# Kernel optimization log

Hardware: AMD Instinct MI355X
Metric: run time of the kernel (lower is better)

## Reference

```python
import jax, jax.numpy as jnp
import numpy as np

DEPTH, DIM, HEADS, EXP = 6, 768, 12, 4
B, N = 8, 1024
EPS = 1e-5


def setup_inputs() -> dict:
    key = jax.random.key(0)
    ks = jax.random.split(key, 6)
    s = 0.02
    inp = {
        "x": jax.random.normal(ks[0], (B, N, DIM), dtype=jnp.float32),
        "ln1_g": jnp.ones((DEPTH, DIM), jnp.float32),
        "ln1_b": jnp.zeros((DEPTH, DIM), jnp.float32),
        "wqkv": jax.random.normal(ks[1], (DEPTH, DIM, 3 * DIM), jnp.float32) * s,
        "bqkv": jnp.zeros((DEPTH, 3 * DIM), jnp.float32),
        "ln2_g": jnp.ones((DEPTH, DIM), jnp.float32),
        "ln2_b": jnp.zeros((DEPTH, DIM), jnp.float32),
        "w1": jax.random.normal(ks[2], (DEPTH, DIM, EXP * DIM), jnp.float32) * s,
        "b1": jnp.zeros((DEPTH, EXP * DIM), jnp.float32),
        "w2": jax.random.normal(ks[3], (DEPTH, EXP * DIM, DIM), jnp.float32) * s,
        "b2": jnp.zeros((DEPTH, DIM), jnp.float32),
    }
    return inp


def _layernorm(x, g, b):
    mu = jnp.mean(x, axis=-1, keepdims=True)
    var = jnp.mean(jnp.square(x - mu), axis=-1, keepdims=True)
    return (x - mu) * jax.lax.rsqrt(var + EPS) * g + b


def _block(x, p):
    ln1_g, ln1_b, wqkv, bqkv, ln2_g, ln2_b, w1, b1, w2, b2 = p
    # --- attention (pre-norm, residual) ---
    x1 = _layernorm(x, ln1_g, ln1_b)
    qkv = x1 @ wqkv + bqkv  # [b, n, 3*dim]
    q, k, v = jnp.split(qkv, 3, axis=-1)
    dh = DIM // HEADS
    def heads(t):  # b n (h d) -> b h n d
        return t.reshape(B, N, HEADS, dh).transpose(0, 2, 1, 3)
    q, k, v = heads(q), heads(k), heads(v)
    scale = DIM ** (-0.5)  # NB: module scales by full dim, not head dim
    dots = jnp.einsum("bhnd,bhmd->bhnm", q, k) * scale
    attn = jax.nn.softmax(dots, axis=-1)
    out = jnp.einsum("bhnm,bhmd->bhnd", attn, v)
    out = out.transpose(0, 2, 1, 3).reshape(B, N, DIM)
    x = x + out
    # --- feedforward (pre-norm, residual) ---
    x2 = _layernorm(x, ln2_g, ln2_b)
    h = jax.nn.gelu(x2 @ w1 + b1, approximate=False)
    x = x + (h @ w2 + b2)
    return x


def reference(x, ln1_g, ln1_b, wqkv, bqkv, ln2_g, ln2_b, w1, b1, w2, b2):
    params = (ln1_g, ln1_b, wqkv, bqkv, ln2_g, ln2_b, w1, b1, w2, b2)

    def body(carry, p):
        return _block(carry, p), None

    x, _ = jax.lax.scan(body, x, params)
    return x
```

## Files before the change

### kernel.cpp

```cpp
#include <hip/hip_runtime.h>
#include <hip/hip_bf16.h>
#include <math.h>

#define DEPTH 6
#define DIM   768
#define HEADS 12
#define DH    64
#define NCTX  1024
#define BATCH 8
#define ROWS  (BATCH*NCTX)
#define DIM3  (3*DIM)
#define DIMF  (4*DIM)
#define LNEPS 1e-5f

typedef __attribute__((ext_vector_type(8))) short short8;
typedef __attribute__((ext_vector_type(4))) float floatx4;
using bf16 = __hip_bfloat16;

static __device__ __forceinline__ bf16 f2bf(float v){ return __float2bfloat16(v); }
static __device__ __forceinline__ float bf2f(unsigned short u){
    union { unsigned int i; float f; } c; c.i = ((unsigned int)u) << 16; return c.f;
}
static __device__ __forceinline__ unsigned short bfu(float v){ return __bfloat16_as_ushort(f2bf(v)); }

static __device__ __forceinline__ void gl_lds16(const void* g, void* l) {
    __builtin_amdgcn_global_load_lds((const __attribute__((address_space(1))) void*)g,
                                     (__attribute__((address_space(3))) void*)l, 16, 0, 0);
}

__global__ void k_transpose_convert(const float* __restrict__ W, bf16* __restrict__ WT,
                                    int K, int N) {
    __shared__ float tile[32][33];
    int l = blockIdx.z;
    const float* Wl = W + (size_t)l * K * N;
    bf16* WTl = WT + (size_t)l * K * N;
    int n0 = blockIdx.x * 32, k0 = blockIdx.y * 32;
    int tx = threadIdx.x, ty = threadIdx.y;
#pragma unroll
    for (int i = 0; i < 4; i++)
        tile[ty + i*8][tx] = Wl[(size_t)(k0 + ty + i*8) * N + n0 + tx];
    __syncthreads();
#pragma unroll
    for (int i = 0; i < 4; i++)
        WTl[(size_t)(n0 + ty + i*8) * K + k0 + tx] = f2bf(tile[tx][ty + i*8]);
}

__global__ __launch_bounds__(256) void k_layernorm(const float* __restrict__ x,
                                                   const float* __restrict__ g,
                                                   const float* __restrict__ b,
                                                   bf16* __restrict__ y) {
    int row  = blockIdx.x * 4 + (threadIdx.x >> 6);
    int lane = threadIdx.x & 63;
    const float4* xr = (const float4*)(x + (size_t)row * DIM);
    float4 v[3];
    float s = 0.f, s2 = 0.f;
#pragma unroll
    for (int i = 0; i < 3; i++) {
        v[i] = xr[lane + i*64];
        s  += v[i].x + v[i].y + v[i].z + v[i].w;
        s2 += v[i].x*v[i].x + v[i].y*v[i].y + v[i].z*v[i].z + v[i].w*v[i].w;
    }
#pragma unroll
    for (int m = 1; m < 64; m <<= 1) { s += __shfl_xor(s, m); s2 += __shfl_xor(s2, m); }
    float mu  = s * (1.f / DIM);
    float var = s2 * (1.f / DIM) - mu * mu;
    float rs  = rsqrtf(var + LNEPS);
    bf16* yr = y + (size_t)row * DIM;
    const float4* g4 = (const float4*)g;
    const float4* b4 = (const float4*)b;
#pragma unroll
    for (int i = 0; i < 3; i++) {
        float4 gg = g4[lane + i*64], bb = b4[lane + i*64];
        float r0 = (v[i].x - mu) * rs * gg.x + bb.x;
        float r1 = (v[i].y - mu) * rs * gg.y + bb.y;
        float r2 = (v[i].z - mu) * rs * gg.z + bb.z;
        float r3 = (v[i].w - mu) * rs * gg.w + bb.w;
        unsigned int lo = bfu(r0) | ((unsigned int)bfu(r1) << 16);
        unsigned int hi = bfu(r2) | ((unsigned int)bfu(r3) << 16);
        uint2 u; u.x = lo; u.y = hi;
        *(uint2*)&yr[4 * (lane + i*64)] = u;
    }
}

template<int MODE>
__global__ __launch_bounds__(256) void k_gemm(const bf16* __restrict__ A,
                                              const bf16* __restrict__ WT,
                                              const float* __restrict__ bias,
                                              bf16* __restrict__ outb,
                                              float* __restrict__ outf,
                                              int N, int K) {
    __shared__ __align__(16) bf16 As[2][128*32];
    __shared__ __align__(16) bf16 Bs[2][128*32];
    int nt = N >> 7;
    int nwg = gridDim.x;
    int fblk = blockIdx.x;
    int swz = (fblk & 7) * (nwg >> 3) + (fblk >> 3);
    int m0 = (swz / nt) * 128, n0 = (swz % nt) * 128;
    int t = threadIdx.x;
    int lane = t & 63, w = t >> 6;
    int wr = (w >> 1) * 64, wc = (w & 1) * 64;
    int lr = lane & 15, lg = lane >> 4;
    int c0 = t, c1 = 256 + t;
    int r0g = c0 >> 2, e0 = (c0 & 3) * 8;
    int r1g = c1 >> 2, e1 = (c1 & 3) * 8;
    const bf16* Arow0 = A  + (size_t)(m0 + r0g) * K + e0;
    const bf16* Arow1 = A  + (size_t)(m0 + r1g) * K + e1;
    const bf16* Brow0 = WT + (size_t)(n0 + r0g) * K + e0;
    const bf16* Brow1 = WT + (size_t)(n0 + r1g) * K + e1;

    floatx4 acc[4][4] = {};
    int NT = K >> 5;
    gl_lds16(Arow0, &As[0][c0 * 8]);
    gl_lds16(Brow0, &Bs[0][c0 * 8]);
    gl_lds16(Arow1, &As[0][c1 * 8]);
    gl_lds16(Brow1, &Bs[0][c1 * 8]);
    __syncthreads();
    int cur = 0;
    for (int ks = 0; ks < NT; ks++) {
        if (ks + 1 < NT) {
            int ko = (ks + 1) << 5;
            gl_lds16(Arow0 + ko, &As[cur^1][c0 * 8]);
            gl_lds16(Brow0 + ko, &Bs[cur^1][c0 * 8]);
            gl_lds16(Arow1 + ko, &As[cur^1][c1 * 8]);
            gl_lds16(Brow1 + ko, &Bs[cur^1][c1 * 8]);
        }
        short8 af[4], bfr[4];
#pragma unroll
        for (int i = 0; i < 4; i++) af[i]  = *(const short8*)&As[cur][(wr + i*16 + lr)*32 + lg*8];
#pragma unroll
        for (int j = 0; j < 4; j++) bfr[j] = *(const short8*)&Bs[cur][(wc + j*16 + lr)*32 + lg*8];
#pragma unroll
        for (int i = 0; i < 4; i++)
#pragma unroll
            for (int j = 0; j < 4; j++)
                acc[i][j] = __builtin_amdgcn_mfma_f32_16x16x32_bf16(af[i], bfr[j], acc[i][j], 0, 0, 0);
        __syncthreads();
        cur ^= 1;
    }
#pragma unroll
    for (int i = 0; i < 4; i++)
#pragma unroll
        for (int j = 0; j < 4; j++)
#pragma unroll
            for (int r = 0; r < 4; r++) {
                int row = m0 + wr + i*16 + lg*4 + r;
                int col = n0 + wc + j*16 + lr;
                float vv = acc[i][j][r] + bias[col];
                if (MODE == 0) {
                    outb[(size_t)row * N + col] = f2bf(vv);
                } else if (MODE == 1) {
                    float u = 1.5957691216f * (vv + 0.044715f * vv * vv * vv);
                    float gs = 1.f / (1.f + __expf(-u));
                    outb[(size_t)row * N + col] = f2bf(vv * gs);
                } else {
                    outf[(size_t)row * N + col] += vv;
                }
            }
}

static __device__ __forceinline__ int vt_off(int d, int k) {
    int dw = d * 36 + (k >> 1);
    dw ^= (d & 0x38) >> 1;
    return dw * 2 + (k & 1);
}

__global__ __launch_bounds__(256, 3) void k_attn(const bf16* __restrict__ qkv,
                                                 float* __restrict__ x) {
    int f = blockIdx.x;
    int b  = f & 7;
    int rr = f >> 3;
    int h  = rr % 12;
    int qt = rr / 12;
    int t = threadIdx.x, lane = t & 63, w = t >> 6;
    int lr = lane & 15, lg = lane >> 4;
    const size_t bn0 = (size_t)b * NCTX;
    const bf16* Qg = qkv + bn0 * DIM3 + h * DH;
    const bf16* Kg = Qg + DIM;
    const bf16* Vg = Qg + 2 * DIM;
    int q0 = qt * 128 + w * 32;

    const float qs = 0.036084391824351615f * 1.4426950408889634f;
    short8 qf[2][2];
#pragma unroll
    for (int i = 0; i < 2; i++)
#pragma unroll
        for (int s = 0; s < 2; s++) {
            short8 raw = *(const short8*)&Qg[(size_t)(q0 + i*16 + lr) * DIM3 + s*32 + lg*8];
            short8 o;
#pragma unroll
            for (int e = 0; e < 8; e++)
                o[e] = (short)bfu(bf2f((unsigned short)raw[e]) * qs);
            qf[i][s] = o;
        }

    __shared__ __align__(16) bf16 Ks[64][72];
    __shared__ __align__(16) bf16 VTs[64 * 72];
    __shared__ __align__(16) bf16 Ps[4][32][72];

    int sr[2], sc[2];
#pragma unroll
    for (int it = 0; it < 2; it++) { int c = it*256 + t; sr[it] = c >> 3; sc[it] = (c & 7) * 8; }

    floatx4 oacc[2][4] = {};
    float mrow[2][4], lrow[2][4];
#pragma unroll
    for (int i = 0; i < 2; i++)
#pragma unroll
        for (int r = 0; r < 4; r++) { mrow[i][r] = -1e30f; lrow[i][r] = 0.f; }

    uint4 kreg[2], vreg[2];
#pragma unroll
    for (int it = 0; it < 2; it++) {
        kreg[it] = *(const uint4*)&Kg[(size_t)sr[it] * DIM3 + sc[it]];
        vreg[it] = *(const uint4*)&Vg[(size_t)sr[it] * DIM3 + sc[it]];
    }

    for (int kt = 0; kt < 16; kt++) {
        __syncthreads();
#pragma unroll
        for (int it = 0; it < 2; it++) {
            *(uint4*)&Ks[sr[it]][sc[it]] = kreg[it];
            const bf16* vp = (const bf16*)&vreg[it];
#pragma unroll
            for (int e = 0; e < 8; e++) VTs[vt_off(sc[it] + e, sr[it])] = vp[e];
        }
        __syncthreads();
        if (kt + 1 < 16) {
            int kv0 = (kt + 1) * 64;
#pragma unroll
            for (int it = 0; it < 2; it++) {
                kreg[it] = *(const uint4*)&Kg[(size_t)(kv0 + sr[it]) * DIM3 + sc[it]];
                vreg[it] = *(const uint4*)&Vg[(size_t)(kv0 + sr[it]) * DIM3 + sc[it]];
            }
        }

        floatx4 sacc[2][4] = {};
#pragma unroll
        for (int j = 0; j < 4; j++) {
            short8 kf0 = *(const short8*)&Ks[j*16 + lr][lg*8];
            short8 kf1 = *(const short8*)&Ks[j*16 + lr][32 + lg*8];
#pragma unroll
            for (int i = 0; i < 2; i++) {
                sacc[i][j] = __builtin_amdgcn_mfma_f32_16x16x32_bf16(qf[i][0], kf0, sacc[i][j], 0, 0, 0);
                sacc[i][j] = __builtin_amdgcn_mfma_f32_16x16x32_bf16(qf[i][1], kf1, sacc[i][j], 0, 0, 0);
            }
        }

#pragma unroll
        for (int i = 0; i < 2; i++)
#pragma unroll
            for (int r = 0; r < 4; r++) {
                float mx = fmaxf(fmaxf(sacc[i][0][r], sacc[i][1][r]),
                                 fmaxf(sacc[i][2][r], sacc[i][3][r]));
#pragma unroll
                for (int m = 1; m < 16; m <<= 1) mx = fmaxf(mx, __shfl_xor(mx, m));
                if (mx > mrow[i][r] + 8.f) {
                    float corr = exp2f(mrow[i][r] - mx);
                    mrow[i][r] = mx;
                    lrow[i][r] *= corr;
#pragma unroll
                    for (int j = 0; j < 4; j++) oacc[i][j][r] *= corr;
                }
                float sum = 0.f;
#pragma unroll
                for (int j = 0; j < 4; j++) {
                    float pv = exp2f(sacc[i][j][r] - mrow[i][r]);
                    sum += pv;
                    Ps[w][i*16 + lg*4 + r][j*16 + lr] = f2bf(pv);
                }
#pragma unroll
                for (int m = 1; m < 16; m <<= 1) sum += __shfl_xor(sum, m);
                lrow[i][r] += sum;
            }

#pragma unroll
        for (int s = 0; s < 2; s++) {
            short8 pa[2];
#pragma unroll
            for (int i = 0; i < 2; i++) pa[i] = *(const short8*)&Ps[w][i*16 + lr][s*32 + lg*8];
#pragma unroll
            for (int j = 0; j < 4; j++) {
                short8 vb = *(const short8*)&VTs[vt_off(j*16 + lr, s*32 + lg*8)];
#pragma unroll
                for (int i = 0; i < 2; i++)
                    oacc[i][j] = __builtin_amdgcn_mfma_f32_16x16x32_bf16(pa[i], vb, oacc[i][j], 0, 0, 0);
            }
        }
    }

    float* xr = x + bn0 * DIM + (size_t)h * DH;
#pragma unroll
    for (int i = 0; i < 2; i++)
#pragma unroll
        for (int j = 0; j < 4; j++)
#pragma unroll
            for (int r = 0; r < 4; r++) {
                int row = q0 + i*16 + lg*4 + r;
                int col = j*16 + lr;
                xr[(size_t)row * DIM + col] += oacc[i][j][r] / lrow[i][r];
            }
}

extern "C" void kernel_launch(void* const* d_in, const int* in_sizes, int n_in,
                              void* d_out, int out_size, void* d_ws, size_t ws_size,
                              hipStream_t stream) {
    const float* x_in  = (const float*)d_in[0];
    const float* ln1_g = (const float*)d_in[1];
    const float* ln1_b = (const float*)d_in[2];
    const float* wqkv  = (const float*)d_in[3];
    const float* bqkv  = (const float*)d_in[4];
    const float* ln2_g = (const float*)d_in[5];
    const float* ln2_b = (const float*)d_in[6];
    const float* w1    = (const float*)d_in[7];
    const float* b1    = (const float*)d_in[8];
    const float* w2    = (const float*)d_in[9];
    const float* b2    = (const float*)d_in[10];
    float* x = (float*)d_out;

    char* ws = (char*)d_ws;
    size_t off = 0;
    auto alloc = [&](size_t bytes) { void* p = ws + off; off += (bytes + 255) & ~255ull; return p; };
    bf16* wqkvT = (bf16*)alloc((size_t)DEPTH * DIM * DIM3 * 2);
    bf16* w1T   = (bf16*)alloc((size_t)DEPTH * DIM * DIMF * 2);
    bf16* w2T   = (bf16*)alloc((size_t)DEPTH * DIMF * DIM * 2);
    bf16* xn    = (bf16*)alloc((size_t)ROWS * DIM * 2);
    bf16* qkvh  = (bf16*)alloc((size_t)ROWS * DIMF * 2);
    if (off > ws_size) return;

    hipMemcpyAsync(x, x_in, (size_t)ROWS * DIM * 4, hipMemcpyDeviceToDevice, stream);

    k_transpose_convert<<<dim3(DIM3/32, DIM/32,  DEPTH), dim3(32, 8), 0, stream>>>(wqkv, wqkvT, DIM,  DIM3);
    k_transpose_convert<<<dim3(DIMF/32, DIM/32,  DEPTH), dim3(32, 8), 0, stream>>>(w1,   w1T,   DIM,  DIMF);
    k_transpose_convert<<<dim3(DIM/32,  DIMF/32, DEPTH), dim3(32, 8), 0, stream>>>(w2,   w2T,   DIMF, DIM);

    for (int l = 0; l < DEPTH; l++) {
        k_layernorm<<<ROWS/4, 256, 0, stream>>>(x, ln1_g + l*DIM, ln1_b + l*DIM, xn);
        k_gemm<0><<<dim3((DIM3/128)*(ROWS/128)), 256, 0, stream>>>(
            xn, wqkvT + (size_t)l*DIM*DIM3, bqkv + (size_t)l*DIM3, qkvh, nullptr, DIM3, DIM);
        k_attn<<<dim3(768), 256, 0, stream>>>(qkvh, x);
        k_layernorm<<<ROWS/4, 256, 0, stream>>>(x, ln2_g + l*DIM, ln2_b + l*DIM, xn);
        k_gemm<1><<<dim3((DIMF/128)*(ROWS/128)), 256, 0, stream>>>(
            xn, w1T + (size_t)l*DIM*DIMF, b1 + (size_t)l*DIMF, qkvh, nullptr, DIMF, DIM);
        k_gemm<2><<<dim3((DIM/128)*(ROWS/128)), 256, 0, stream>>>(
            qkvh, w2T + (size_t)l*DIMF*DIM, b2 + (size_t)l*DIM, nullptr, x, DIM, DIMF);
    }
}
```

Before: 1.785 ms.

## Rewrite attention with 32x32x16 MFMA and transposed score layout

Moves the flash-attention kernel from 16x16x32 MFMA tiles to 32x32x16 tiles. It computes S^T (K as the A operand) so each lane owns one query column, which cuts the row max and sum reductions to a single cross-half shuffle. K and P are stored in XOR-swizzled LDS to avoid bank conflicts. The online-softmax correction factors are broadcast through a small shared buffer so they can be applied to the output accumulator layout. This adds LDS traffic and layout complexity, and it relies on intra-wave ordering of the shared writes and reads with no barrier.

Measured after the change: 1.648 ms. -7.7%, faster.

```diff
diff --git a/kernel.cpp b/kernel.cpp
--- a/kernel.cpp
+++ b/kernel.cpp
@@ -13,15 +13,20 @@
 #define DIMF  (4*DIM)
 #define LNEPS 1e-5f
 
-typedef __attribute__((ext_vector_type(8))) short short8;
-typedef __attribute__((ext_vector_type(4))) float floatx4;
+typedef __attribute__((ext_vector_type(8)))  short short8;
+typedef __attribute__((ext_vector_type(4)))  float floatx4;
+typedef __attribute__((ext_vector_type(16))) float floatx16;
 using bf16 = __hip_bfloat16;
+typedef unsigned int u32;
 
 static __device__ __forceinline__ bf16 f2bf(float v){ return __float2bfloat16(v); }
 static __device__ __forceinline__ float bf2f(unsigned short u){
     union { unsigned int i; float f; } c; c.i = ((unsigned int)u) << 16; return c.f;
 }
 static __device__ __forceinline__ unsigned short bfu(float v){ return __bfloat16_as_ushort(f2bf(v)); }
+static __device__ __forceinline__ u32 pk2(float a, float b){
+    return (u32)bfu(a) | ((u32)bfu(b) << 16);
+}
 
 static __device__ __forceinline__ void gl_lds16(const void* g, void* l) {
     __builtin_amdgcn_global_load_lds((const __attribute__((address_space(1))) void*)g,
@@ -75,9 +80,7 @@
         float r1 = (v[i].y - mu) * rs * gg.y + bb.y;
         float r2 = (v[i].z - mu) * rs * gg.z + bb.z;
         float r3 = (v[i].w - mu) * rs * gg.w + bb.w;
-        unsigned int lo = bfu(r0) | ((unsigned int)bfu(r1) << 16);
-        unsigned int hi = bfu(r2) | ((unsigned int)bfu(r3) << 16);
-        uint2 u; u.x = lo; u.y = hi;
+        uint2 u; u.x = pk2(r0, r1); u.y = pk2(r2, r3);
         *(uint2*)&yr[4 * (lane + i*64)] = u;
     }
 }
@@ -172,7 +175,7 @@
     int h  = rr % 12;
     int qt = rr / 12;
     int t = threadIdx.x, lane = t & 63, w = t >> 6;
-    int lr = lane & 15, lg = lane >> 4;
+    int q = lane & 31, hi = lane >> 5;
     const size_t bn0 = (size_t)b * NCTX;
     const bf16* Qg = qkv + bn0 * DIM3 + h * DH;
     const bf16* Kg = Qg + DIM;
@@ -180,33 +183,31 @@
     int q0 = qt * 128 + w * 32;
 
     const float qs = 0.036084391824351615f * 1.4426950408889634f;
-    short8 qf[2][2];
-#pragma unroll
-    for (int i = 0; i < 2; i++)
-#pragma unroll
-        for (int s = 0; s < 2; s++) {
-            short8 raw = *(const short8*)&Qg[(size_t)(q0 + i*16 + lr) * DIM3 + s*32 + lg*8];
-            short8 o;
-#pragma unroll
-            for (int e = 0; e < 8; e++)
-                o[e] = (short)bfu(bf2f((unsigned short)raw[e]) * qs);
-            qf[i][s] = o;
-        }
-
-    __shared__ __align__(16) bf16 Ks[64][72];
-    __shared__ __align__(16) bf16 VTs[64 * 72];
-    __shared__ __align__(16) bf16 Ps[4][32][72];
+    short8 qf[4];
+#pragma unroll
+    for (int s = 0; s < 4; s++) {
+        short8 raw = *(const short8*)&Qg[(size_t)(q0 + q) * DIM3 + s*16 + hi*8];
+        short8 o;
+#pragma unroll
+        for (int e = 0; e < 8; e++)
+            o[e] = (short)bfu(bf2f((unsigned short)raw[e]) * qs);
+        qf[s] = o;
+    }
+
+    __shared__ __align__(16) bf16 KsS[64*64];
+    __shared__ __align__(16) bf16 VTs[64*72];
+    __shared__ __align__(16) bf16 PsS[4][32*64];
+    __shared__ float wbc[4][32];
+
+    u32* ksw = (u32*)KsS;
+    u32* psw = (u32*)&PsS[w][0];
 
     int sr[2], sc[2];
 #pragma unroll
     for (int it = 0; it < 2; it++) { int c = it*256 + t; sr[it] = c >> 3; sc[it] = (c & 7) * 8; }
 
-    floatx4 oacc[2][4] = {};
-    float mrow[2][4], lrow[2][4];
-#pragma unroll
-    for (int i = 0; i < 2; i++)
-#pragma unroll
-        for (int r = 0; r < 4; r++) { mrow[i][r] = -1e30f; lrow[i][r] = 0.f; }
+    floatx16 pacc[2] = {};
+    float mrow = -3e38f, lrow = 0.f;
 
     uint4 kreg[2], vreg[2];
 #pragma unroll
@@ -219,10 +220,11 @@
         __syncthreads();
 #pragma unroll
         for (int it = 0; it < 2; it++) {
-            *(uint4*)&Ks[sr[it]][sc[it]] = kreg[it];
+            int row = sr[it], u = sc[it] >> 3;
+            *(uint4*)(ksw + row*32 + ((u ^ (row & 7)) << 2)) = kreg[it];
             const bf16* vp = (const bf16*)&vreg[it];
 #pragma unroll
-            for (int e = 0; e < 8; e++) VTs[vt_off(sc[it] + e, sr[it])] = vp[e];
+            for (int e = 0; e < 8; e++) VTs[vt_off(sc[it] + e, row)] = vp[e];
         }
         __syncthreads();
         if (kt + 1 < 16) {
@@ -234,71 +236,76 @@
             }
         }
 
-        floatx4 sacc[2][4] = {};
-#pragma unroll
-        for (int j = 0; j < 4; j++) {
-            short8 kf0 = *(const short8*)&Ks[j*16 + lr][lg*8];
-            short8 kf1 = *(const short8*)&Ks[j*16 + lr][32 + lg*8];
-#pragma unroll
-            for (int i = 0; i < 2; i++) {
-                sacc[i][j] = __builtin_amdgcn_mfma_f32_16x16x32_bf16(qf[i][0], kf0, sacc[i][j], 0, 0, 0);
-                sacc[i][j] = __builtin_amdgcn_mfma_f32_16x16x32_bf16(qf[i][1], kf1, sacc[i][j], 0, 0, 0);
-            }
-        }
-
-#pragma unroll
-        for (int i = 0; i < 2; i++)
-#pragma unroll
-            for (int r = 0; r < 4; r++) {
-                float mx = fmaxf(fmaxf(sacc[i][0][r], sacc[i][1][r]),
-                                 fmaxf(sacc[i][2][r], sacc[i][3][r]));
-#pragma unroll
-                for (int m = 1; m < 16; m <<= 1) mx = fmaxf(mx, __shfl_xor(mx, m));
-                if (mx > mrow[i][r] + 8.f) {
-                    float corr = exp2f(mrow[i][r] - mx);
-                    mrow[i][r] = mx;
-                    lrow[i][r] *= corr;
-#pragma unroll
-                    for (int j = 0; j < 4; j++) oacc[i][j][r] *= corr;
-                }
-                float sum = 0.f;
-#pragma unroll
-                for (int j = 0; j < 4; j++) {
-                    float pv = exp2f(sacc[i][j][r] - mrow[i][r]);
-                    sum += pv;
-                    Ps[w][i*16 + lg*4 + r][j*16 + lr] = f2bf(pv);
-                }
-#pragma unroll
-                for (int m = 1; m < 16; m <<= 1) sum += __shfl_xor(sum, m);
-                lrow[i][r] += sum;
-            }
-
-#pragma unroll
-        for (int s = 0; s < 2; s++) {
-            short8 pa[2];
-#pragma unroll
-            for (int i = 0; i < 2; i++) pa[i] = *(const short8*)&Ps[w][i*16 + lr][s*32 + lg*8];
-#pragma unroll
-            for (int j = 0; j < 4; j++) {
-                short8 vb = *(const short8*)&VTs[vt_off(j*16 + lr, s*32 + lg*8)];
-#pragma unroll
-                for (int i = 0; i < 2; i++)
-                    oacc[i][j] = __builtin_amdgcn_mfma_f32_16x16x32_bf16(pa[i], vb, oacc[i][j], 0, 0, 0);
-            }
-        }
-    }
-
+        floatx16 sacc[2] = {};
+#pragma unroll
+        for (int kb = 0; kb < 2; kb++) {
+#pragma unroll
+            for (int s = 0; s < 4; s++) {
+                int row = kb*32 + q;
+                short8 kf = *(const short8*)(ksw + row*32 + (((2*s + hi) ^ (row & 7)) << 2));
+                sacc[kb] = __builtin_amdgcn_mfma_f32_32x32x16_bf16(kf, qf[s], sacc[kb], 0, 0, 0);
+            }
+        }
+
+        float mx = sacc[0][0];
+#pragma unroll
+        for (int r = 1; r < 16; r++) mx = fmaxf(mx, sacc[0][r]);
+#pragma unroll
+        for (int r = 0; r < 16; r++) mx = fmaxf(mx, sacc[1][r]);
+        mx = fmaxf(mx, __shfl_xor(mx, 32));
+        bool chg = mx > mrow + 8.f;
+        if (__any(chg)) {
+            float mnew = chg ? mx : mrow;
+            float corr = exp2f(mrow - mnew);
+            mrow = mnew;
+            lrow *= corr;
+            wbc[w][q] = corr;
+#pragma unroll
+            for (int r = 0; r < 16; r++) {
+                float c = wbc[w][(r & 3) + 8*(r >> 2) + 4*hi];
+                pacc[0][r] *= c; pacc[1][r] *= c;
+            }
+        }
+        float sum = 0.f;
+#pragma unroll
+        for (int kb = 0; kb < 2; kb++) {
+#pragma unroll
+            for (int m = 0; m < 4; m++) {
+                float p0 = exp2f(sacc[kb][4*m+0] - mrow);
+                float p1 = exp2f(sacc[kb][4*m+1] - mrow);
+                float p2 = exp2f(sacc[kb][4*m+2] - mrow);
+                float p3 = exp2f(sacc[kb][4*m+3] - mrow);
+                sum += (p0 + p1) + (p2 + p3);
+                uint2 d2; d2.x = pk2(p0, p1); d2.y = pk2(p2, p3);
+                *(uint2*)(psw + q*32 + (((m + 4*kb) ^ (q & 7)) << 2) + 2*hi) = d2;
+            }
+        }
+        sum += __shfl_xor(sum, 32);
+        lrow += sum;
+
+#pragma unroll
+        for (int ks = 0; ks < 4; ks++) {
+            short8 pa = *(const short8*)(psw + q*32 + (((2*ks + hi) ^ (q & 7)) << 2));
+#pragma unroll
+            for (int db = 0; db < 2; db++) {
+                short8 vb = *(const short8*)&VTs[vt_off(db*32 + q, 16*ks + 8*hi)];
+                pacc[db] = __builtin_amdgcn_mfma_f32_32x32x16_bf16(pa, vb, pacc[db], 0, 0, 0);
+            }
+        }
+    }
+
+    wbc[w][q] = 1.f / lrow;
     float* xr = x + bn0 * DIM + (size_t)h * DH;
 #pragma unroll
-    for (int i = 0; i < 2; i++)
-#pragma unroll
-        for (int j = 0; j < 4; j++)
-#pragma unroll
-            for (int r = 0; r < 4; r++) {
-                int row = q0 + i*16 + lg*4 + r;
-                int col = j*16 + lr;
-                xr[(size_t)row * DIM + col] += oacc[i][j][r] / lrow[i][r];
-            }
+    for (int r = 0; r < 16; r++) {
+        int qrow = (r & 3) + 8*(r >> 2) + 4*hi;
+        float li = wbc[w][qrow];
+#pragma unroll
+        for (int db = 0; db < 2; db++) {
+            int col = db*32 + q;
+            xr[(size_t)(q0 + qrow) * DIM + col] += pacc[db][r] * li;
+        }
+    }
 }
 
 extern "C" void kernel_launch(void* const* d_in, const int* in_sizes, int n_in,
```
